# Kernel tuning notes

Hardware: AMD Instinct MI355X
Metric: run time of the kernel (lower is better)

Reference implementation:

```python
import jax, jax.numpy as jnp
import numpy as np

DIM = 2048
LAT = 512          # dim / compression_factor
NH = 16
NKV = 4
HD = LAT // NH     # 32
KVD = NKV * HD     # 128
K = 3              # conv kernel
GAIN = 0.25
EPS = 1e-6
THETA = 10000.0


def _rms(x, g):
    x32 = x.astype(jnp.float32)
    r = jax.lax.rsqrt(jnp.mean(x32 * x32, axis=-1, keepdims=True) + EPS)
    return (x32 * r).astype(x.dtype) * g.astype(x.dtype)


def _causal_conv(x, w, groups):
    # x: [B,S,C], w: [C, C//groups, K]; left-pad K-1 == pad both + trim right
    xc = jnp.transpose(x, (0, 2, 1))
    y = jax.lax.conv_general_dilated(
        xc, w, window_strides=(1,), padding=[(K - 1, 0)],
        feature_group_count=groups, dimension_numbers=('NCH', 'OIH', 'NCH'))
    return jnp.transpose(y, (0, 2, 1))


def _rope_tables(S):
    freqs = 1.0 / THETA ** (jnp.arange(0, HD, 2, dtype=jnp.float32) / HD)
    t = jnp.arange(S, dtype=jnp.float32)
    f = jnp.outer(t, freqs)               # [S, HD/2]
    return jnp.cos(f), jnp.sin(f)


def _rope(x, cos, sin):
    # x: [B,H,S,HD]; interleaved even/odd rotation
    x1, x2 = x[..., ::2], x[..., 1::2]
    r1 = x1 * cos - x2 * sin
    r2 = x1 * sin + x2 * cos
    return jnp.stack([r1, r2], axis=-1).reshape(x.shape)


def setup_inputs() -> dict:
    key = jax.random.key(0)
    ks = jax.random.split(key, 8)
    s = 0.02
    return {
        'x': jax.random.normal(ks[0], (4, 2048, DIM), jnp.float32),
        'w_q': jax.random.normal(ks[1], (LAT, DIM), jnp.float32) * s,
        'w_k': jax.random.normal(ks[2], (KVD, DIM), jnp.float32) * s,
        'w_v': jax.random.normal(ks[3], (KVD, DIM), jnp.float32) * s,
        'g_latent': jnp.ones((LAT,), jnp.float32),
        'g_kv': jnp.ones((KVD,), jnp.float32),
        'conv_q_w': jax.random.normal(ks[4], (LAT, LAT // NH, K), jnp.float32) * s,
        'conv_k_w': jax.random.normal(ks[5], (KVD, KVD // NKV, K), jnp.float32) * s,
        'g_conv': jnp.ones((LAT,), jnp.float32),
        'g_kconv': jnp.ones((KVD,), jnp.float32),
        'g_postq': jnp.ones((LAT,), jnp.float32),
        'g_postk': jnp.ones((KVD,), jnp.float32),
        'key_temp': jnp.ones((1,), jnp.float32),
        'g_preout': jnp.ones((LAT,), jnp.float32),
        'w_o': jax.random.normal(ks[6], (DIM, LAT), jnp.float32) * s,
    }


def reference(x, w_q, w_k, w_v, g_latent, g_kv, conv_q_w, conv_k_w,
              g_conv, g_kconv, g_postq, g_postk, key_temp, g_preout, w_o):
    B, S, D = x.shape
    n_groups = NH // NKV

    q = _rms(x @ w_q.T, g_latent)          # [B,S,LAT]
    k = _rms(x @ w_k.T, g_kv)              # [B,S,KVD]
    v = _rms(x @ w_v.T, g_kv)
    q_pre, k_pre = q, k

    q = _rms(_causal_conv(q, conv_q_w, NH), g_conv)
    k = _rms(_causal_conv(k, conv_k_w, NKV), g_kconv)

    # qk-mean modulation (n_groups > 1 branch)
    q_mean = q_pre.reshape(B, S, NH, HD).mean(axis=2)    # [B,S,HD]
    k_mean = k_pre.reshape(B, S, NKV, HD).mean(axis=2)   # [B,S,HD]
    q = q + GAIN * jnp.broadcast_to(k_mean[:, :, None, :], (B, S, NH, HD)).reshape(B, S, LAT)
    k = k + GAIN * jnp.broadcast_to(q_mean[:, :, None, :], (B, S, NKV, HD)).reshape(B, S, KVD)

    q = _rms(q, g_postq)
    k = _rms(k, g_postk)

    q = q.reshape(B, S, NH, HD).transpose(0, 2, 1, 3)    # [B,NH,S,HD]
    k = k.reshape(B, S, NKV, HD).transpose(0, 2, 1, 3)   # [B,NKV,S,HD]
    v = v.reshape(B, S, NKV, HD).transpose(0, 2, 1, 3)

    # QK L2 norm with learnable key temperature
    sqrt_hd = jnp.sqrt(jnp.float32(HD))
    qn = jnp.maximum(jnp.linalg.norm(q, axis=-1, keepdims=True), 1e-12)
    kn = jnp.maximum(jnp.linalg.norm(k, axis=-1, keepdims=True), 1e-12)
    q = q / qn * sqrt_hd
    k = k / kn * sqrt_hd * key_temp[0]

    cos, sin = _rope_tables(S)
    q = _rope(q, cos, sin)
    k = _rope(k, cos, sin)

    # GQA expand kv heads
    k = jnp.broadcast_to(k[:, :, None], (B, NKV, n_groups, S, HD)).reshape(B, NH, S, HD)
    v = jnp.broadcast_to(v[:, :, None], (B, NKV, n_groups, S, HD)).reshape(B, NH, S, HD)

    scale = HD ** -0.5
    scores = jnp.einsum('bhqd,bhkd->bhqk', q, k) * scale
    causal = jnp.tril(jnp.ones((S, S), bool))
    scores = jnp.where(causal, scores, jnp.finfo(scores.dtype).min)
    attn = jax.nn.softmax(scores, axis=-1)
    out = jnp.einsum('bhqk,bhkd->bhqd', attn, v)

    out = out.transpose(0, 2, 1, 3).reshape(B, S, LAT)
    out = _rms(out, g_preout)
    return out @ w_o.T
```

## Files before the change

kernel.cpp:

```cpp
#include <hip/hip_runtime.h>
#include <hip/hip_bf16.h>
#include <math.h>

constexpr int S_LEN = 2048;
constexpr int B_SZ  = 4;
constexpr int NROWS = B_SZ * S_LEN;
constexpr float GAIN_  = 0.25f;
constexpr float EPS_   = 1e-6f;
constexpr float THETA_ = 10000.0f;
constexpr float LOG2E_ = 1.44269504f;

typedef __attribute__((ext_vector_type(8))) short short8;
typedef __attribute__((ext_vector_type(4))) short sshort4;
typedef __attribute__((ext_vector_type(4))) float float4v;

__device__ __forceinline__ short f2bs(float f) {
    __hip_bfloat16 h = __float2bfloat16(f);
    short r;
    __builtin_memcpy(&r, &h, 2);
    return r;
}

__device__ __forceinline__ void async_copy16(const short* g, short* l) {
    __builtin_amdgcn_global_load_lds(
        (const __attribute__((address_space(1))) void*)g,
        (__attribute__((address_space(3))) void*)l, 16, 0, 0);
}

__device__ __forceinline__ float block_reduce_sum_256(float v, float* scratch) {
    __syncthreads();
    for (int off = 32; off > 0; off >>= 1)
        v += __shfl_down(v, off, 64);
    int lane = threadIdx.x & 63;
    int wid  = threadIdx.x >> 6;
    if (lane == 0) scratch[wid] = v;
    __syncthreads();
    return scratch[0] + scratch[1] + scratch[2] + scratch[3];
}

__device__ __forceinline__ void block_reduce_sum2_256(float& a, float& b, float* scratch) {
    __syncthreads();
    for (int off = 32; off > 0; off >>= 1) {
        a += __shfl_down(a, off, 64);
        b += __shfl_down(b, off, 64);
    }
    int lane = threadIdx.x & 63;
    int wid  = threadIdx.x >> 6;
    if (lane == 0) { scratch[wid] = a; scratch[4 + wid] = b; }
    __syncthreads();
    a = scratch[0] + scratch[1] + scratch[2] + scratch[3];
    b = scratch[4] + scratch[5] + scratch[6] + scratch[7];
}

__device__ __forceinline__ void block_reduce_sum3_256(float& a, float& b, float& c, float* scratch) {
    __syncthreads();
    for (int off = 32; off > 0; off >>= 1) {
        a += __shfl_down(a, off, 64);
        b += __shfl_down(b, off, 64);
        c += __shfl_down(c, off, 64);
    }
    int lane = threadIdx.x & 63;
    int wid  = threadIdx.x >> 6;
    if (lane == 0) { scratch[wid] = a; scratch[4 + wid] = b; scratch[8 + wid] = c; }
    __syncthreads();
    a = scratch[0] + scratch[1] + scratch[2] + scratch[3];
    b = scratch[4] + scratch[5] + scratch[6] + scratch[7];
    c = scratch[8] + scratch[9] + scratch[10] + scratch[11];
}

__global__ __launch_bounds__(256) void cvt_bf16(
    const float* __restrict__ src, short* __restrict__ dst, int n) {
    int i = (blockIdx.x * 256 + threadIdx.x) * 4;
    if (i >= n) return;
    float4 v = *(const float4*)(src + i);
    sshort4 o;
    o.x = f2bs(v.x); o.y = f2bs(v.y); o.z = f2bs(v.z); o.w = f2bs(v.w);
    *(sshort4*)(dst + i) = o;
}

__global__ __launch_bounds__(256) void cvt_weights(
    const float* __restrict__ wq, const float* __restrict__ wk,
    const float* __restrict__ wv, const float* __restrict__ wo,
    short* __restrict__ wqkvb, short* __restrict__ wob) {
    int i = (blockIdx.x * 256 + threadIdx.x) * 4;
    const float* src;
    short* dst;
    int j;
    if (i < 1048576)      { src = wq; dst = wqkvb + i; j = i; }
    else if (i < 1310720) { src = wk; dst = wqkvb + i; j = i - 1048576; }
    else if (i < 1572864) { src = wv; dst = wqkvb + i; j = i - 1310720; }
    else                  { src = wo; dst = wob + (i - 1572864); j = i - 1572864; }
    float4 v = *(const float4*)(src + j);
    sshort4 o;
    o.x = f2bs(v.x); o.y = f2bs(v.y); o.z = f2bs(v.z); o.w = f2bs(v.w);
    *(sshort4*)dst = o;
}

__global__ __launch_bounds__(256) void gemm_bf16_mfma(
    const short* __restrict__ A, const short* __restrict__ B,
    float* __restrict__ C, int N, int K) {
    __shared__ short As[128 * 32];
    __shared__ short Bs[128 * 32];
    int tid = threadIdx.x;
    int wave = tid >> 6, lane = tid & 63;
    int m0 = blockIdx.y * 128, n0 = blockIdx.x * 128;
    int wm = (wave >> 1) * 64, wn = (wave & 1) * 64;
    int mrow = lane & 15, quad = lane >> 4;
    float4v acc[4][4] = {};
    for (int k0 = 0; k0 < K; k0 += 32) {
        __syncthreads();
#pragma unroll
        for (int p = 0; p < 2; ++p) {
            int f = p * 256 + tid;
            int row = f >> 2, ch = (f & 3) * 8;
            const short* ga = A + (size_t)(m0 + row) * K + k0 + ch;
            const short* gb = B + (size_t)(n0 + row) * K + k0 + ch;
            async_copy16(ga, As + p * 2048 + wave * 512);
            async_copy16(gb, Bs + p * 2048 + wave * 512);
        }
        __syncthreads();
        short8 af[4], bf[4];
#pragma unroll
        for (int i = 0; i < 4; ++i)
            af[i] = *(const short8*)&As[(wm + i * 16 + mrow) * 32 + quad * 8];
#pragma unroll
        for (int j = 0; j < 4; ++j)
            bf[j] = *(const short8*)&Bs[(wn + j * 16 + mrow) * 32 + quad * 8];
#pragma unroll
        for (int i = 0; i < 4; ++i)
#pragma unroll
            for (int j = 0; j < 4; ++j)
                acc[i][j] = __builtin_amdgcn_mfma_f32_16x16x32_bf16(af[i], bf[j], acc[i][j], 0, 0, 0);
    }
#pragma unroll
    for (int i = 0; i < 4; ++i)
#pragma unroll
        for (int r = 0; r < 4; ++r) {
            int m = m0 + wm + i * 16 + quad * 4 + r;
            float* crow = C + (size_t)m * N + n0 + wn;
#pragma unroll
            for (int j = 0; j < 4; ++j)
                crow[j * 16 + mrow] = acc[i][j][r];
        }
}

__global__ __launch_bounds__(256) void rms_qkv_means(
    float* __restrict__ qkv, const float* __restrict__ g_latent,
    const float* __restrict__ g_kv,
    float* __restrict__ qmean, float* __restrict__ kmean,
    short* __restrict__ vtb) {
    int row = blockIdx.x;
    int b = row >> 11, s = row & (S_LEN - 1);
    float* p = qkv + (size_t)row * 768;
    __shared__ float sh[640];
    __shared__ float scratch[12];
    int tid = threadIdx.x;
    float v0 = p[tid], v1 = p[tid + 256], v2 = p[tid + 512];
    float sq = v0 * v0 + v1 * v1;
    float sk = (tid < 128) ? v2 * v2 : 0.f;
    float sv = (tid >= 128) ? v2 * v2 : 0.f;
    block_reduce_sum3_256(sq, sk, sv, scratch);
    float rq = rsqrtf(sq / 512.f + EPS_);
    float q0 = v0 * rq * g_latent[tid];
    float q1 = v1 * rq * g_latent[tid + 256];
    p[tid] = q0; p[tid + 256] = q1;
    sh[tid] = q0; sh[tid + 256] = q1;
    if (tid < 128) {
        float rk = rsqrtf(sk / 128.f + EPS_);
        float kv = v2 * rk * g_kv[tid];
        p[512 + tid] = kv; sh[512 + tid] = kv;
    } else {
        float rv = rsqrtf(sv / 128.f + EPS_);
        float vv = v2 * rv * g_kv[tid - 128];
        int d_full = tid - 128;
        vtb[((size_t)(b * 4 + (d_full >> 5)) * 32 + (d_full & 31)) * S_LEN + s] = f2bs(vv);
    }
    __syncthreads();
    if (tid < 32) {
        float sm = 0.f;
#pragma unroll
        for (int h = 0; h < 16; ++h) sm += sh[h * 32 + tid];
        qmean[(size_t)row * 32 + tid] = sm * (1.f / 16.f);
    } else if (tid < 64) {
        int d = tid - 32;
        float sm = 0.f;
#pragma unroll
        for (int h = 0; h < 4; ++h) sm += sh[512 + h * 32 + d];
        kmean[(size_t)row * 32 + d] = sm * 0.25f;
    }
}

__global__ __launch_bounds__(256) void causal_conv32(
    const float* __restrict__ in, int ldin, int inoff,
    const float* __restrict__ w, float* __restrict__ out, int C) {
    int b = blockIdx.z, g = blockIdx.y, s0 = blockIdx.x * 32;
    __shared__ float wsh[32][3][32];
    __shared__ float ish[34][33];
    int tid = threadIdx.x;
    for (int i = tid; i < 32 * 96; i += 256) {
        int oc = i / 96, r = i % 96;
        wsh[r / 3][r % 3][oc] = w[(size_t)(g * 32 + oc) * 96 + r];
    }
    for (int i = tid; i < 34 * 32; i += 256) {
        int pp = i >> 5, ic = i & 31;
        int s = s0 - 2 + pp;
        ish[pp][ic] = (s >= 0) ? in[((size_t)b * S_LEN + s) * ldin + inoff + g * 32 + ic] : 0.f;
    }
    __syncthreads();
    int sl = tid >> 3, oc0 = (tid & 7) * 4;
    float acc[4] = {0.f, 0.f, 0.f, 0.f};
    for (int ic = 0; ic < 32; ++ic) {
        float x0 = ish[sl][ic], x1 = ish[sl + 1][ic], x2 = ish[sl + 2][ic];
#pragma unroll
        for (int j = 0; j < 4; ++j)
            acc[j] += x0 * wsh[ic][0][oc0 + j] + x1 * wsh[ic][1][oc0 + j] + x2 * wsh[ic][2][oc0 + j];
    }
    float* orow = out + ((size_t)b * S_LEN + s0 + sl) * C + g * 32 + oc0;
    orow[0] = acc[0]; orow[1] = acc[1]; orow[2] = acc[2]; orow[3] = acc[3];
}

__global__ __launch_bounds__(256) void mix_rows(
    const float* __restrict__ convq, const float* __restrict__ convk,
    const float* __restrict__ qmean, const float* __restrict__ kmean,
    const float* __restrict__ g_conv, const float* __restrict__ g_kconv,
    const float* __restrict__ g_postq, const float* __restrict__ g_postk,
    const float* __restrict__ key_temp,
    short* __restrict__ qb, short* __restrict__ kb) {
    int row = blockIdx.x;
    int s = row & (S_LEN - 1);
    int tid = threadIdx.x;
    __shared__ float sh[640];
    __shared__ float scratch[8];
    __shared__ float hscale[20];
    float q0 = convq[(size_t)row * 512 + tid];
    float q1 = convq[(size_t)row * 512 + tid + 256];
    float k0 = (tid < 128) ? convk[(size_t)row * 128 + tid] : 0.f;
    float ssq = q0 * q0 + q1 * q1;
    float ssk = k0 * k0;
    block_reduce_sum2_256(ssq, ssk, scratch);
    float r1  = rsqrtf(ssq / 512.f + EPS_);
    float rk1 = rsqrtf(ssk / 128.f + EPS_);
    float km = kmean[(size_t)row * 32 + (tid & 31)];
    float a0 = q0 * r1 * g_conv[tid] + GAIN_ * km;
    float a1 = q1 * r1 * g_conv[tid + 256] + GAIN_ * km;
    float ak = 0.f;
    if (tid < 128) ak = k0 * rk1 * g_kconv[tid] + GAIN_ * qmean[(size_t)row * 32 + (tid & 31)];
    float ssq2 = a0 * a0 + a1 * a1;
    float ssk2 = ak * ak;
    block_reduce_sum2_256(ssq2, ssk2, scratch);
    float r2  = rsqrtf(ssq2 / 512.f + EPS_);
    float rk2 = rsqrtf(ssk2 / 128.f + EPS_);
    sh[tid] = a0 * r2 * g_postq[tid];
    sh[tid + 256] = a1 * r2 * g_postq[tid + 256];
    if (tid < 128) sh[512 + tid] = ak * rk2 * g_postk[tid];
    __syncthreads();
    if (tid < 16) {
        float ssh = 0.f;
        for (int d = 0; d < 32; ++d) { float x = sh[tid * 32 + d]; ssh += x * x; }
        hscale[tid] = 1.f / fmaxf(sqrtf(ssh), 1e-12f);
    } else if (tid < 20) {
        int h = tid - 16;
        float ssh = 0.f;
        for (int d = 0; d < 32; ++d) { float x = sh[512 + h * 32 + d]; ssh += x * x; }
        hscale[tid] = sqrtf(32.f) / fmaxf(sqrtf(ssh), 1e-12f) * key_temp[0];
    }
    __syncthreads();
    {
        int i0 = tid * 2;
        int h = i0 >> 5;
        int fi = (i0 & 31) >> 1;
        float sc = hscale[h];
        float x1 = sh[i0] * sc, x2 = sh[i0 + 1] * sc;
        float freq = powf(THETA_, -(float)fi / 16.f);
        float ang = (float)s * freq;
        float sn, cs;
        sincosf(ang, &sn, &cs);
        unsigned lo = (unsigned short)f2bs(x1 * cs - x2 * sn);
        unsigned hi = (unsigned short)f2bs(x1 * sn + x2 * cs);
        *(unsigned*)(qb + (size_t)row * 512 + i0) = lo | (hi << 16);
    }
    if (tid < 64) {
        int i0 = tid * 2;
        int h = i0 >> 5;
        int fi = (i0 & 31) >> 1;
        float sc = hscale[16 + h];
        float x1 = sh[512 + i0] * sc, x2 = sh[512 + i0 + 1] * sc;
        float freq = powf(THETA_, -(float)fi / 16.f);
        float ang = (float)s * freq;
        float sn, cs;
        sincosf(ang, &sn, &cs);
        unsigned lo = (unsigned short)f2bs(x1 * cs - x2 * sn);
        unsigned hi = (unsigned short)f2bs(x1 * sn + x2 * cs);
        *(unsigned*)(kb + (size_t)row * 128 + i0) = lo | (hi << 16);
    }
}

__global__ __launch_bounds__(256) void attn_mfma(
    const short* __restrict__ qb, const short* __restrict__ kb,
    const short* __restrict__ vtb, float* __restrict__ OnumA,
    float* __restrict__ OnumB, float* __restrict__ LsumA,
    float* __restrict__ LsumB, const float* __restrict__ key_temp) {
    int pp = blockIdx.x, h = blockIdx.y, b = blockIdx.z;
    int pair = pp >> 1, parity = pp & 1;
    int kvh = h >> 2;
    float* __restrict__ Onum = parity ? OnumB : OnumA;
    float* __restrict__ Lsum = parity ? LsumB : LsumA;
    __shared__ short KF[2][2048];
    __shared__ short VF[2][2048];
    __shared__ __align__(16) short PF[4 * 16 * 72];
    int tid = threadIdx.x, wave = tid >> 6, lane = tid & 63;
    int cc = lane & 15, quad = lane >> 4;
    short* PFw = PF + wave * 16 * 72;
    int ldsoff = wave * 512;
    float shift2 = -5.6568543f * key_temp[0] * LOG2E_;

    const short* ksrc0 = kb +
        ((size_t)(b * S_LEN + parity * 64 + wave * 16 + (tid & 15)) * 128
         + kvh * 32 + ((tid >> 4) & 3) * 8);
    const short* vsrc0 = vtb +
        ((size_t)((b * 4 + kvh) * 32 + (wave & 1) * 16 + (tid & 15)) * S_LEN
         + parity * 64 + (tid >> 7) * 32 + ((tid >> 4) & 3) * 8);

    for (int half = 0; half < 2; ++half) {
        int qt = half ? (31 - pair) : pair;
        int s0 = qt * 64;
        short8 qfrag = *(const short8*)(qb +
            ((size_t)(b * S_LEN + s0 + wave * 16 + cc) * 512 + h * 32 + quad * 8));
        float4v accO[2];
        accO[0] = (float4v){0.f, 0.f, 0.f, 0.f};
        accO[1] = (float4v){0.f, 0.f, 0.f, 0.f};
        float lpart = 0.f;
        int qpos = s0 + wave * 16 + cc;
        const short* ksrc = ksrc0;
        const short* vsrc = vsrc0;
        int nkt = (qt - parity + 2) >> 1;

        __syncthreads();
        int cur = 0;
        if (nkt > 0) {
            async_copy16(ksrc, KF[0] + ldsoff);
            async_copy16(vsrc, VF[0] + ldsoff);
            ksrc += 2 * 64 * 128;
            vsrc += 2 * 64;
        }
        for (int it = 0; it < nkt; ++it) {
            int kt = parity + it * 2;
            __syncthreads();
            if (it + 1 < nkt) {
                async_copy16(ksrc, KF[cur ^ 1] + ldsoff);
                async_copy16(vsrc, VF[cur ^ 1] + ldsoff);
                ksrc += 2 * 64 * 128;
                vsrc += 2 * 64;
            }
            const short* KFc = KF[cur];
            const short* VFc = VF[cur];

            float4v st[4];
#pragma unroll
            for (int chunk = 0; chunk < 4; ++chunk) {
                short8 kfrag = *(const short8*)&KFc[chunk * 512 + lane * 8];
                float4v z = (float4v){0.f, 0.f, 0.f, 0.f};
                st[chunk] = __builtin_amdgcn_mfma_f32_16x16x32_bf16(kfrag, qfrag, z, 0, 0, 0);
            }

            bool diag = (kt == qt);
#pragma unroll
            for (int chunk = 0; chunk < 4; ++chunk) {
                float pv[4];
#pragma unroll
                for (int r = 0; r < 4; ++r) {
                    float e = exp2f(fmaf(st[chunk][r], LOG2E_, shift2));
                    if (diag) {
                        int kpos = kt * 64 + chunk * 16 + quad * 4 + r;
                        e = (kpos <= qpos) ? e : 0.f;
                    }
                    pv[r] = e;
                    lpart += e;
                }
                unsigned a0 = __float_as_uint(pv[0]) + 0x8000u;
                unsigned a1 = __float_as_uint(pv[1]) + 0x8000u;
                unsigned a2 = __float_as_uint(pv[2]) + 0x8000u;
                unsigned a3 = __float_as_uint(pv[3]) + 0x8000u;
                unsigned u0 = __builtin_amdgcn_perm(a1, a0, 0x07060302);
                unsigned u1 = __builtin_amdgcn_perm(a3, a2, 0x07060302);
                *(uint2*)&PFw[cc * 72 + chunk * 16 + quad * 4] = make_uint2(u0, u1);
            }

#pragma unroll
            for (int kc = 0; kc < 2; ++kc) {
                short8 pfrag = *(const short8*)&PFw[cc * 72 + kc * 32 + quad * 8];
#pragma unroll
                for (int dc = 0; dc < 2; ++dc) {
                    short8 vfrag = *(const short8*)&VFc[(kc * 2 + dc) * 512 + lane * 8];
                    accO[dc] = __builtin_amdgcn_mfma_f32_16x16x32_bf16(pfrag, vfrag, accO[dc], 0, 0, 0);
                }
            }
            cur ^= 1;
        }

        lpart += __shfl_xor(lpart, 16, 64);
        lpart += __shfl_xor(lpart, 32, 64);
        if (quad == 0)
            Lsum[((size_t)(b * S_LEN + s0 + wave * 16 + cc)) * 16 + h] = lpart;
#pragma unroll
        for (int r = 0; r < 4; ++r) {
            float* dst = Onum +
                ((size_t)(b * S_LEN + s0 + wave * 16 + quad * 4 + r) * 512 + h * 32 + cc);
            dst[0]  = accO[0][r];
            dst[16] = accO[1][r];
        }
    }
}

__global__ __launch_bounds__(256) void rms_preout_bf16(
    const float* __restrict__ OA, const float* __restrict__ OB,
    const float* __restrict__ LA, const float* __restrict__ LB,
    const float* __restrict__ g, short* __restrict__ outb) {
    int row = blockIdx.x;
    __shared__ float scratch[4];
    __shared__ float linv[16];
    int tid = threadIdx.x;
    if (tid < 16)
        linv[tid] = 1.f / (LA[(size_t)row * 16 + tid] + LB[(size_t)row * 16 + tid]);
    __syncthreads();
    float v0 = (OA[(size_t)row * 512 + tid] + OB[(size_t)row * 512 + tid]) * linv[tid >> 5];
    float v1 = (OA[(size_t)row * 512 + tid + 256] + OB[(size_t)row * 512 + tid + 256])
               * linv[(tid + 256) >> 5];
    float ssq = block_reduce_sum_256(v0 * v0 + v1 * v1, scratch);
    float r = rsqrtf(ssq / 512.f + EPS_);
    outb[(size_t)row * 512 + tid]       = f2bs(v0 * r * g[tid]);
    outb[(size_t)row * 512 + tid + 256] = f2bs(v1 * r * g[tid + 256]);
}

extern "C" void kernel_launch(void* const* d_in, const int* in_sizes, int n_in,
                              void* d_out, int out_size, void* d_ws, size_t ws_size,
                              hipStream_t stream) {
    (void)in_sizes; (void)n_in; (void)out_size; (void)ws_size;
    const float* x        = (const float*)d_in[0];
    const float* w_q      = (const float*)d_in[1];
    const float* w_k      = (const float*)d_in[2];
    const float* w_v      = (const float*)d_in[3];
    const float* g_latent = (const float*)d_in[4];
    const float* g_kv     = (const float*)d_in[5];
    const float* conv_q_w = (const float*)d_in[6];
    const float* conv_k_w = (const float*)d_in[7];
    const float* g_conv   = (const float*)d_in[8];
    const float* g_kconv  = (const float*)d_in[9];
    const float* g_postq  = (const float*)d_in[10];
    const float* g_postk  = (const float*)d_in[11];
    const float* key_temp = (const float*)d_in[12];
    const float* g_preout = (const float*)d_in[13];
    const float* w_o      = (const float*)d_in[14];
    float* out = (float*)d_out;

    char* ws = (char*)d_ws;
    const size_t R = NROWS;
    float* qkv   = (float*)ws;                        ws += R * 768 * 4;
    float* qmean = (float*)ws;                        ws += R * 32 * 4;
    float* kmean = (float*)ws;                        ws += R * 32 * 4;
    float* convq = (float*)ws;                        ws += R * 512 * 4;
    float* convk = (float*)ws;                        ws += R * 128 * 4;
    short* qbb   = (short*)ws;                        ws += R * 512 * 2;
    short* kbb   = (short*)ws;                        ws += R * 128 * 2;
    short* vtb   = (short*)ws;                        ws += R * 128 * 2;
    short* xb    = (short*)ws;                        ws += R * 2048 * 2;
    short* wqkvb = (short*)ws;                        ws += 768 * 2048 * 2;
    short* w_ob  = (short*)ws;                        ws += 2048 * 512 * 2;
    float* OnumA = convq;
    float* OnumB = qkv;
    float* LsumA = qmean;
    float* LsumB = kmean;
    short* attnb = xb;

    dim3 blk(256);
    cvt_bf16<<<(NROWS * 2048) / 1024, blk, 0, stream>>>(x, xb, NROWS * 2048);
    cvt_weights<<<2560, blk, 0, stream>>>(w_q, w_k, w_v, w_o, wqkvb, w_ob);

    gemm_bf16_mfma<<<dim3(6, 64), blk, 0, stream>>>(xb, wqkvb, qkv, 768, 2048);
    rms_qkv_means<<<NROWS, blk, 0, stream>>>(qkv, g_latent, g_kv, qmean, kmean, vtb);
    causal_conv32<<<dim3(64, 16, 4), blk, 0, stream>>>(qkv, 768, 0, conv_q_w, convq, 512);
    causal_conv32<<<dim3(64, 4, 4), blk, 0, stream>>>(qkv, 768, 512, conv_k_w, convk, 128);
    mix_rows<<<NROWS, blk, 0, stream>>>(convq, convk, qmean, kmean, g_conv, g_kconv,
                                        g_postq, g_postk, key_temp, qbb, kbb);
    attn_mfma<<<dim3(32, 16, 4), blk, 0, stream>>>(qbb, kbb, vtb, OnumA, OnumB,
                                                   LsumA, LsumB, key_temp);
    rms_preout_bf16<<<NROWS, blk, 0, stream>>>(OnumA, OnumB, LsumA, LsumB,
                                               g_preout, attnb);
    gemm_bf16_mfma<<<dim3(16, 64), blk, 0, stream>>>(attnb, w_ob, out, 2048, 512);
}
```

Before: 394.1 us.

## Split-K the QKV GEMM and streamline attention exp and row-sum

Result: faster. 383.2 us (-2.8%).

```diff
diff --git a/kernel.cpp b/kernel.cpp
--- a/kernel.cpp
+++ b/kernel.cpp
@@ -144,18 +144,72 @@
         }
 }
 
+__global__ __launch_bounds__(256) void gemm_bf16_mfma_sk2(
+    const short* __restrict__ A, const short* __restrict__ B,
+    float* __restrict__ C0, float* __restrict__ C1, int N, int K) {
+    __shared__ short As[128 * 32];
+    __shared__ short Bs[128 * 32];
+    int tid = threadIdx.x;
+    int wave = tid >> 6, lane = tid & 63;
+    int m0 = blockIdx.y * 128, n0 = blockIdx.x * 128;
+    int wm = (wave >> 1) * 64, wn = (wave & 1) * 64;
+    int mrow = lane & 15, quad = lane >> 4;
+    int kh = K >> 1;
+    int kbeg = blockIdx.z * kh, kend = kbeg + kh;
+    float* __restrict__ C = blockIdx.z ? C1 : C0;
+    float4v acc[4][4] = {};
+    for (int k0 = kbeg; k0 < kend; k0 += 32) {
+        __syncthreads();
+#pragma unroll
+        for (int p = 0; p < 2; ++p) {
+            int f = p * 256 + tid;
+            int row = f >> 2, ch = (f & 3) * 8;
+            const short* ga = A + (size_t)(m0 + row) * K + k0 + ch;
+            const short* gb = B + (size_t)(n0 + row) * K + k0 + ch;
+            async_copy16(ga, As + p * 2048 + wave * 512);
+            async_copy16(gb, Bs + p * 2048 + wave * 512);
+        }
+        __syncthreads();
+        short8 af[4], bf[4];
+#pragma unroll
+        for (int i = 0; i < 4; ++i)
+            af[i] = *(const short8*)&As[(wm + i * 16 + mrow) * 32 + quad * 8];
+#pragma unroll
+        for (int j = 0; j < 4; ++j)
+            bf[j] = *(const short8*)&Bs[(wn + j * 16 + mrow) * 32 + quad * 8];
+#pragma unroll
+        for (int i = 0; i < 4; ++i)
+#pragma unroll
+            for (int j = 0; j < 4; ++j)
+                acc[i][j] = __builtin_amdgcn_mfma_f32_16x16x32_bf16(af[i], bf[j], acc[i][j], 0, 0, 0);
+    }
+#pragma unroll
+    for (int i = 0; i < 4; ++i)
+#pragma unroll
+        for (int r = 0; r < 4; ++r) {
+            int m = m0 + wm + i * 16 + quad * 4 + r;
+            float* crow = C + (size_t)m * N + n0 + wn;
+#pragma unroll
+            for (int j = 0; j < 4; ++j)
+                crow[j * 16 + mrow] = acc[i][j][r];
+        }
+}
+
 __global__ __launch_bounds__(256) void rms_qkv_means(
-    float* __restrict__ qkv, const float* __restrict__ g_latent,
-    const float* __restrict__ g_kv,
+    float* __restrict__ qkv, const float* __restrict__ qkv2,
+    const float* __restrict__ g_latent, const float* __restrict__ g_kv,
     float* __restrict__ qmean, float* __restrict__ kmean,
     short* __restrict__ vtb) {
     int row = blockIdx.x;
     int b = row >> 11, s = row & (S_LEN - 1);
     float* p = qkv + (size_t)row * 768;
+    const float* p2 = qkv2 + (size_t)row * 768;
     __shared__ float sh[640];
     __shared__ float scratch[12];
     int tid = threadIdx.x;
-    float v0 = p[tid], v1 = p[tid + 256], v2 = p[tid + 512];
+    float v0 = p[tid] + p2[tid];
+    float v1 = p[tid + 256] + p2[tid + 256];
+    float v2 = p[tid + 512] + p2[tid + 512];
     float sq = v0 * v0 + v1 * v1;
     float sk = (tid < 128) ? v2 * v2 : 0.f;
     float sv = (tid >= 128) ? v2 * v2 : 0.f;
@@ -257,7 +311,7 @@
     if (tid < 16) {
         float ssh = 0.f;
         for (int d = 0; d < 32; ++d) { float x = sh[tid * 32 + d]; ssh += x * x; }
-        hscale[tid] = 1.f / fmaxf(sqrtf(ssh), 1e-12f);
+        hscale[tid] = LOG2E_ / fmaxf(sqrtf(ssh), 1e-12f);
     } else if (tid < 20) {
         int h = tid - 16;
         float ssh = 0.f;
@@ -313,6 +367,10 @@
     short* PFw = PF + wave * 16 * 72;
     int ldsoff = wave * 512;
     float shift2 = -5.6568543f * key_temp[0] * LOG2E_;
+    float4v zinit = {shift2, shift2, shift2, shift2};
+    short8 ones;
+#pragma unroll
+    for (int j = 0; j < 8; ++j) ones[j] = (short)0x3F80;
 
     const short* ksrc0 = kb +
         ((size_t)(b * S_LEN + parity * 64 + wave * 16 + (tid & 15)) * 128
@@ -329,7 +387,7 @@
         float4v accO[2];
         accO[0] = (float4v){0.f, 0.f, 0.f, 0.f};
         accO[1] = (float4v){0.f, 0.f, 0.f, 0.f};
-        float lpart = 0.f;
+        float4v accL = (float4v){0.f, 0.f, 0.f, 0.f};
         int qpos = s0 + wave * 16 + cc;
         const short* ksrc = ksrc0;
         const short* vsrc = vsrc0;
@@ -359,8 +417,7 @@
 #pragma unroll
             for (int chunk = 0; chunk < 4; ++chunk) {
                 short8 kfrag = *(const short8*)&KFc[chunk * 512 + lane * 8];
-                float4v z = (float4v){0.f, 0.f, 0.f, 0.f};
-                st[chunk] = __builtin_amdgcn_mfma_f32_16x16x32_bf16(kfrag, qfrag, z, 0, 0, 0);
+                st[chunk] = __builtin_amdgcn_mfma_f32_16x16x32_bf16(kfrag, qfrag, zinit, 0, 0, 0);
             }
 
             bool diag = (kt == qt);
@@ -369,26 +426,23 @@
                 float pv[4];
 #pragma unroll
                 for (int r = 0; r < 4; ++r) {
-                    float e = exp2f(fmaf(st[chunk][r], LOG2E_, shift2));
+                    float e = exp2f(st[chunk][r]);
                     if (diag) {
                         int kpos = kt * 64 + chunk * 16 + quad * 4 + r;
                         e = (kpos <= qpos) ? e : 0.f;
                     }
                     pv[r] = e;
-                    lpart += e;
                 }
-                unsigned a0 = __float_as_uint(pv[0]) + 0x8000u;
-                unsigned a1 = __float_as_uint(pv[1]) + 0x8000u;
-                unsigned a2 = __float_as_uint(pv[2]) + 0x8000u;
-                unsigned a3 = __float_as_uint(pv[3]) + 0x8000u;
-                unsigned u0 = __builtin_amdgcn_perm(a1, a0, 0x07060302);
-                unsigned u1 = __builtin_amdgcn_perm(a3, a2, 0x07060302);
+                unsigned u0, u1;
+                asm("v_cvt_pk_bf16_f32 %0, %1, %2" : "=v"(u0) : "v"(pv[0]), "v"(pv[1]));
+                asm("v_cvt_pk_bf16_f32 %0, %1, %2" : "=v"(u1) : "v"(pv[2]), "v"(pv[3]));
                 *(uint2*)&PFw[cc * 72 + chunk * 16 + quad * 4] = make_uint2(u0, u1);
             }
 
 #pragma unroll
             for (int kc = 0; kc < 2; ++kc) {
                 short8 pfrag = *(const short8*)&PFw[cc * 72 + kc * 32 + quad * 8];
+                accL = __builtin_amdgcn_mfma_f32_16x16x32_bf16(pfrag, ones, accL, 0, 0, 0);
 #pragma unroll
                 for (int dc = 0; dc < 2; ++dc) {
                     short8 vfrag = *(const short8*)&VFc[(kc * 2 + dc) * 512 + lane * 8];
@@ -398,10 +452,11 @@
             cur ^= 1;
         }
 
-        lpart += __shfl_xor(lpart, 16, 64);
-        lpart += __shfl_xor(lpart, 32, 64);
-        if (quad == 0)
-            Lsum[((size_t)(b * S_LEN + s0 + wave * 16 + cc)) * 16 + h] = lpart;
+        if (cc == 0) {
+#pragma unroll
+            for (int r = 0; r < 4; ++r)
+                Lsum[((size_t)(b * S_LEN + s0 + wave * 16 + quad * 4 + r)) * 16 + h] = accL[r];
+        }
 #pragma unroll
         for (int r = 0; r < 4; ++r) {
             float* dst = Onum +
@@ -466,6 +521,7 @@
     short* xb    = (short*)ws;                        ws += R * 2048 * 2;
     short* wqkvb = (short*)ws;                        ws += 768 * 2048 * 2;
     short* w_ob  = (short*)ws;                        ws += 2048 * 512 * 2;
+    float* qkv2  = convq;
     float* OnumA = convq;
     float* OnumB = qkv;
     float* LsumA = qmean;
@@ -476,8 +532,8 @@
     cvt_bf16<<<(NROWS * 2048) / 1024, blk, 0, stream>>>(x, xb, NROWS * 2048);
     cvt_weights<<<2560, blk, 0, stream>>>(w_q, w_k, w_v, w_o, wqkvb, w_ob);
 
-    gemm_bf16_mfma<<<dim3(6, 64), blk, 0, stream>>>(xb, wqkvb, qkv, 768, 2048);
-    rms_qkv_means<<<NROWS, blk, 0, stream>>>(qkv, g_latent, g_kv, qmean, kmean, vtb);
+    gemm_bf16_mfma_sk2<<<dim3(6, 64, 2), blk, 0, stream>>>(xb, wqkvb, qkv, qkv2, 768, 2048);
+    rms_qkv_means<<<NROWS, blk, 0, stream>>>(qkv, qkv2, g_latent, g_kv, qmean, kmean, vtb);
     causal_conv32<<<dim3(64, 16, 4), blk, 0, stream>>>(qkv, 768, 0, conv_q_w, convq, 512);
     causal_conv32<<<dim3(64, 4, 4), blk, 0, stream>>>(qkv, 768, 512, conv_k_w, convk, 128);
     mix_rows<<<NROWS, blk, 0, stream>>>(convq, convk, qmean, kmean, g_conv, g_kconv,
```
